# Optimization experiments

Measured on AMD Instinct MI355X. Metric: run time of the kernel, lower is better.

Reference implementation:

```python
import jax, jax.numpy as jnp
import numpy as np

TOP_K = 6
CAP_FACTOR = 2.0


def setup_inputs() -> dict:
    key = jax.random.key(0)
    ks = jax.random.split(key, 9)
    B, S, D, F, E, SH = 4, 2048, 512, 256, 64, 2
    return {
        "x": jax.random.normal(ks[0], (B, S, D), jnp.float32),
        "router_w": jax.random.normal(ks[1], (E, D), jnp.float32) * 0.02,
        "bias": jnp.zeros((E,), jnp.float32),
        "shared_w_gate": jax.random.normal(ks[2], (SH, F, D), jnp.float32) * 0.02,
        "shared_w_up": jax.random.normal(ks[3], (SH, F, D), jnp.float32) * 0.02,
        "shared_w_down": jax.random.normal(ks[4], (SH, D, F), jnp.float32) * 0.02,
        "w_gate": jax.random.normal(ks[5], (E, F, D), jnp.float32) * 0.02,
        "w_up": jax.random.normal(ks[6], (E, F, D), jnp.float32) * 0.02,
        "w_down": jax.random.normal(ks[7], (E, D, F), jnp.float32) * 0.02,
    }


def reference(x, router_w, bias, shared_w_gate, shared_w_up, shared_w_down, w_gate, w_up, w_down):
    B, S, D = x.shape
    E = router_w.shape[0]
    K = TOP_K
    N = B * S
    C = max(1, int(N * K * CAP_FACTOR / E))  # static per-expert capacity

    # Router logits with balancing bias (loop_idx=0 row).
    router_logits = jnp.einsum('bsd,ed->bse', x, router_w) + bias

    # Shared experts: averaged SwiGLU over SH experts, fully batched.
    hg = jnp.einsum('bsd,efd->bsef', x, shared_w_gate)
    hu = jnp.einsum('bsd,efd->bsef', x, shared_w_up)
    shared_out = jnp.einsum('bsef,edf->bsd', jax.nn.silu(hg) * hu, shared_w_down)
    shared_out = shared_out / shared_w_gate.shape[0]

    # Top-k routing, renormalised gates.
    router_probs = jax.nn.softmax(router_logits, axis=-1)
    topk_p, topk_i = jax.lax.top_k(router_probs, K)  # [B,S,K]
    topk_p = topk_p / (jnp.sum(topk_p, axis=-1, keepdims=True) + 1e-9)

    x_flat = x.reshape(N, D)
    flat_e = topk_i.reshape(-1)            # [N*K] expert ids
    flat_g = topk_p.reshape(-1)            # [N*K] gates
    token_ids = jnp.repeat(jnp.arange(N), K)

    # Stable sort by expert id -> contiguous expert groups.
    order = jnp.argsort(flat_e)            # jax argsort is stable
    se = flat_e[order]
    st = token_ids[order]
    sg = flat_g[order]

    M = se.shape[0]
    pos = jnp.arange(M)
    is_first = jnp.concatenate([jnp.ones((1,), bool), se[1:] != se[:-1]])
    group_starts = jax.lax.cummax(pos * is_first.astype(pos.dtype))
    slot = pos - group_starts              # position within expert group
    valid = slot < C                       # capacity drop
    safe_slot = jnp.where(valid, slot, C)  # overflow -> scratch slot C

    # Static-shape dispatch buffers (E, C+1, ...); slot C is scratch.
    expert_in = jnp.zeros((E, C + 1, D), x.dtype).at[se, safe_slot].set(x_flat[st])
    expert_gate = jnp.zeros((E, C + 1), x.dtype).at[se, safe_slot].set(sg)
    expert_tok = jnp.full((E, C + 1), N, jnp.int32).at[se, safe_slot].set(st.astype(jnp.int32))
    expert_mask = jnp.zeros((E, C + 1), bool).at[se, safe_slot].set(valid)

    expert_in = expert_in[:, :C]
    expert_gate = expert_gate[:, :C]
    expert_tok = expert_tok[:, :C]
    expert_mask = expert_mask[:, :C]

    # Grouped SwiGLU: three batched GEMMs over experts.
    hg = jnp.einsum('ecd,efd->ecf', expert_in, w_gate)
    hu = jnp.einsum('ecd,efd->ecf', expert_in, w_up)
    expert_out = jnp.einsum('ecf,edf->ecd', jax.nn.silu(hg) * hu, w_down)

    # Combine: scatter-add gated outputs back to tokens; row N is a sink.
    fm = expert_mask.reshape(-1)
    dst = jnp.where(fm, expert_tok.reshape(-1), N)
    fg = jnp.where(fm, expert_gate.reshape(-1), jnp.zeros((), x.dtype))
    sparse = jax.ops.segment_sum(fg[:, None] * expert_out.reshape(-1, D), dst, num_segments=N + 1)[:N]

    return shared_out + sparse.reshape(B, S, D)
```

## Files before the change

### kernel.cpp

```cpp
#include <hip/hip_runtime.h>
#include <hip/hip_bf16.h>
#include <math.h>

#define N_TOK 8192
#define D_DIM 512
#define F_DIM 256
#define E_NUM 64
#define SH_NUM 2
#define K_TOP 6
#define CAP   1536
#define M_ENT (N_TOK * K_TOP)
#define NCHUNK (M_ENT / 256)

#define EW_STRIDE 393216
#define E_TOT (E_NUM + SH_NUM)
#define X_BF_BYTES   (8388608ull)
#define WT_BYTES     ((size_t)E_TOT * EW_STRIDE * 2)
#define TOK_ROUTED   (E_NUM * CAP)
#define TOK_TOTAL    (TOK_ROUTED + SH_NUM * N_TOK)
#define EO_BYTES     ((size_t)TOK_TOTAL * D_DIM * 2)
#define RWT_BYTES    131072ull

#define SLOT 20480

typedef __attribute__((ext_vector_type(8))) short bf16x8;
typedef __attribute__((ext_vector_type(8))) short short8;
typedef __attribute__((ext_vector_type(4))) float f32x4;

#define VMCNT(n) asm volatile("s_waitcnt vmcnt(" #n ")" ::: "memory")

__device__ __forceinline__ ushort f2bf(float f) {
  union { float f; unsigned u; } c; c.f = f;
  return (ushort)((c.u + 0x7FFFu + ((c.u >> 16) & 1u)) >> 16);
}
__device__ __forceinline__ float bf2f(ushort h) {
  union { unsigned u; float f; } c; c.u = ((unsigned)h) << 16;
  return c.f;
}
__device__ __forceinline__ void gload16(const void* g, void* l) {
  __builtin_amdgcn_global_load_lds(
      (const __attribute__((address_space(1))) void*)g,
      (__attribute__((address_space(3))) void*)l, 16, 0, 0);
}

__global__ void router_topk(const float* __restrict__ x, const float* __restrict__ rw,
                            const float* __restrict__ bias, int* __restrict__ topk_i,
                            float* __restrict__ topk_p) {
  const int wave = threadIdx.x >> 6;
  const int lane = threadIdx.x & 63;
  const int n = blockIdx.x * 4 + wave;
  if (n >= N_TOK) return;

  const float4* xr = (const float4*)(x + (size_t)n * D_DIM);
  const float4* wr = (const float4*)(rw + (size_t)lane * D_DIM);
  float acc = 0.f;
  #pragma unroll 4
  for (int d4 = 0; d4 < D_DIM / 4; ++d4) {
    float4 xv = xr[d4]; float4 wv = wr[d4];
    acc += xv.x * wv.x + xv.y * wv.y + xv.z * wv.z + xv.w * wv.w;
  }
  float logit = acc + bias[lane];

  float m = logit;
  for (int off = 32; off > 0; off >>= 1) m = fmaxf(m, __shfl_xor(m, off));
  float p = expf(logit - m);
  float s = p;
  for (int off = 32; off > 0; off >>= 1) s += __shfl_xor(s, off);
  float prob = p / s;

  float myp = prob;
  float gsum = 0.f;
  float myg = 0.f; int myi = -1;
  for (int k = 0; k < K_TOP; ++k) {
    float bp = myp; int bi = lane;
    for (int off = 32; off > 0; off >>= 1) {
      float op = __shfl_xor(bp, off); int oi = __shfl_xor(bi, off);
      if (op > bp || (op == bp && oi < bi)) { bp = op; bi = oi; }
    }
    gsum += bp;
    if (lane == k) { myg = bp; myi = bi; }
    if (lane == bi) myp = -1.f;
  }
  if (lane < K_TOP) {
    topk_i[n * K_TOP + lane] = myi;
    topk_p[n * K_TOP + lane] = myg / (gsum + 1e-9f);
  }
}

__device__ __forceinline__ void softmax_topk_write(float logit, int n, int lane,
                                                   int* __restrict__ topk_i,
                                                   float* __restrict__ topk_p) {
  float m = logit;
  for (int off = 32; off > 0; off >>= 1) m = fmaxf(m, __shfl_xor(m, off));
  float p = expf(logit - m);
  float s = p;
  for (int off = 32; off > 0; off >>= 1) s += __shfl_xor(s, off);
  float prob = p / s;

  float myp = prob;
  float gsum = 0.f;
  float myg = 0.f; int myi = -1;
  #pragma unroll 1
  for (int k = 0; k < K_TOP; ++k) {
    float bp = myp; int bi = lane;
    for (int off = 32; off > 0; off >>= 1) {
      float op = __shfl_xor(bp, off); int oi = __shfl_xor(bi, off);
      if (op > bp || (op == bp && oi < bi)) { bp = op; bi = oi; }
    }
    gsum += bp;
    if (lane == k) { myg = bp; myi = bi; }
    if (lane == bi) myp = -1.f;
  }
  if (lane < K_TOP) {
    topk_i[n * K_TOP + lane] = myi;
    topk_p[n * K_TOP + lane] = myg / (gsum + 1e-9f);
  }
}

__global__ void __launch_bounds__(256) router_topk2(
    const float* __restrict__ x, const float* __restrict__ rwt,
    const float* __restrict__ bias, int* __restrict__ topk_i,
    float* __restrict__ topk_p) {
  const int wave = threadIdx.x >> 6;
  const int lane = threadIdx.x & 63;
  const int n0 = blockIdx.x * 32 + wave * 8;

  float acc[8];
  #pragma unroll
  for (int t = 0; t < 8; ++t) acc[t] = 0.f;

  const float4* wv4 = (const float4*)rwt;
  #pragma unroll 2
  for (int k4 = 0; k4 < 128; ++k4) {
    float4 w = wv4[k4 * 64 + lane];
    #pragma unroll
    for (int t = 0; t < 8; ++t) {
      float4 xv = *(const float4*)(x + (size_t)(n0 + t) * D_DIM + k4 * 4);
      acc[t] += xv.x * w.x + xv.y * w.y + xv.z * w.z + xv.w * w.w;
    }
  }
  float b = bias[lane];
  #pragma unroll 1
  for (int t = 0; t < 8; ++t)
    softmax_topk_write(acc[t] + b, n0 + t, lane, topk_i, topk_p);
}

__global__ void hist_kernel(const int* __restrict__ topk_i, int* __restrict__ chunk_hist) {
  __shared__ int h[E_NUM];
  const int tid = threadIdx.x;
  if (tid < E_NUM) h[tid] = 0;
  __syncthreads();
  int e = topk_i[blockIdx.x * 256 + tid];
  atomicAdd(&h[e], 1);
  __syncthreads();
  if (tid < E_NUM) chunk_hist[blockIdx.x * E_NUM + tid] = h[tid];
}

__global__ void scan_kernel(const int* __restrict__ chunk_hist, int* __restrict__ chunk_base) {
  const int e = threadIdx.x;
  int run = 0;
  for (int c = 0; c < NCHUNK; ++c) {
    chunk_base[c * E_NUM + e] = run;
    run += chunk_hist[c * E_NUM + e];
  }
}

__global__ void dispatch_kernel(const int* __restrict__ topk_i, const float* __restrict__ topk_p,
                                const int* __restrict__ chunk_base,
                                int* __restrict__ expert_tok, float* __restrict__ expert_gate,
                                int* __restrict__ entry_row) {
  __shared__ int eid[256];
  const int tid = threadIdx.x;
  const int m = blockIdx.x * 256 + tid;
  const int e = topk_i[m];
  eid[tid] = e;
  __syncthreads();
  int rank = 0;
  for (int t = 0; t < tid; ++t) rank += (eid[t] == e);
  int slot = chunk_base[blockIdx.x * E_NUM + e] + rank;
  int row = -1;
  if (slot < CAP) {
    expert_tok[e * CAP + slot] = m / K_TOP;
    expert_gate[e * CAP + slot] = topk_p[m];
    row = e * CAP + slot;
  }
  if (entry_row) entry_row[m] = row;
}


__global__ void convert_x_misc(const float* __restrict__ x, ushort* __restrict__ xb,
                               const float* __restrict__ rw, float* __restrict__ rwt,
                               int* __restrict__ tok_all, float* __restrict__ gate_all) {
  int b = blockIdx.x;
  if (b < 2048) {
    size_t idx = (size_t)b * 256 + threadIdx.x;
    const float4* s4 = (const float4*)(x + idx * 8);
    float4 v0 = s4[0], v1 = s4[1];
    short8 o;
    o[0] = f2bf(v0.x); o[1] = f2bf(v0.y); o[2] = f2bf(v0.z); o[3] = f2bf(v0.w);
    o[4] = f2bf(v1.x); o[5] = f2bf(v1.y); o[6] = f2bf(v1.z); o[7] = f2bf(v1.w);
    *(short8*)(xb + idx * 8) = o;
  } else if (b < 2080) {
    int idx = (b - 2048) * 256 + threadIdx.x;
    int e = idx >> 7, k4 = idx & 127;
    float4 v = *(const float4*)(rw + (size_t)e * D_DIM + k4 * 4);
    *(float4*)(rwt + ((size_t)k4 * 64 + e) * 4) = v;
  } else {
    int i = (b - 2080) * 256 + threadIdx.x;
    tok_all[TOK_ROUTED + i] = i & (N_TOK - 1);
    gate_all[TOK_ROUTED + i] = 0.5f;
  }
}

__global__ void convert_w(const float* __restrict__ wg_, const float* __restrict__ wu_,
                          const float* __restrict__ wd_, const float* __restrict__ swg,
                          const float* __restrict__ swu, const float* __restrict__ swd,
                          ushort* __restrict__ Wt) {
  int e = blockIdx.x / 12;
  int rem = blockIdx.x - e * 12;
  int p = rem >> 2, q = rem & 3;
  const float* src;
  if (p == 0)      src = (e < E_NUM) ? wg_ + (size_t)e * 131072 : swg + (size_t)(e - E_NUM) * 131072;
  else if (p == 1) src = (e < E_NUM) ? wu_ + (size_t)e * 131072 : swu + (size_t)(e - E_NUM) * 131072;
  else             src = (e < E_NUM) ? wd_ + (size_t)e * 131072 : swd + (size_t)(e - E_NUM) * 131072;
  ushort* dst = Wt + (size_t)e * EW_STRIDE + (size_t)p * 131072;
  #pragma unroll
  for (int i = 0; i < 16; ++i) {
    int d = q * 32768 + i * 2048 + threadIdx.x * 8;
    int ci = d >> 13;
    int r  = d & 8191;
    int nt = r >> 9;
    int rr = r & 511;
    int k8 = rr >> 7;
    int n  = nt * 16 + ((rr >> 3) & 15);
    size_t srcidx;
    if (p < 2) {
      srcidx = (size_t)n * 512 + ci * 32 + k8 * 8;
    } else {
      int np = ci >> 3, kc = ci & 7;
      srcidx = (size_t)(np * 256 + n) * 256 + kc * 32 + k8 * 8;
    }
    const float4* s4 = (const float4*)(src + srcidx);
    float4 v0 = s4[0], v1 = s4[1];
    short8 o;
    o[0] = f2bf(v0.x); o[1] = f2bf(v0.y); o[2] = f2bf(v0.z); o[3] = f2bf(v0.w);
    o[4] = f2bf(v1.x); o[5] = f2bf(v1.y); o[6] = f2bf(v1.z); o[7] = f2bf(v1.w);
    *(short8*)(dst + d) = o;
  }
}

template <bool GATHER>
__global__ void __launch_bounds__(512, 1) ffn_mfma(
    const ushort* __restrict__ xb, const ushort* __restrict__ Wt,
    const int* __restrict__ tok_all, const float* __restrict__ gate_all,
    float* __restrict__ out, ushort* __restrict__ expert_out) {
  int e, tbase;
  {
    int xcd = blockIdx.x & 7;
    int j = blockIdx.x >> 3;
    if (j < 96) {
      int ec = j / 12;
      int mt = j - ec * 12;
      e = ec * 8 + xcd;
      tbase = e * CAP + mt * 128;
      if (tok_all[tbase] < 0) return;
    } else {
      int s = xcd * 16 + (j - 96);
      int sh = s & 1, mt = s >> 1;
      e = E_NUM + sh;
      tbase = TOK_ROUTED + sh * N_TOK + mt * 128;
    }
  }
  const ushort* wbase = Wt + (size_t)e * EW_STRIDE;

  __shared__ ushort RING[2 * SLOT];
  __shared__ ushort Act[32768];
  __shared__ int   toks[128];
  __shared__ float gts[128];

  const int tid = threadIdx.x;
  const int lane = tid & 63;
  const int wid = tid >> 6;
  const int wr = wid >> 2;
  const int wc = wid & 3;
  const int rl = lane & 15;
  const int hi = lane >> 4;

  if (tid < 128) {
    int t = tok_all[tbase + tid];
    toks[tid] = t;
    gts[tid] = (t >= 0) ? gate_all[tbase + tid] : 0.f;
  }
  __syncthreads();

  int t0 = toks[wid * 16 + rl];
  const ushort* xsrc = xb + (size_t)(t0 < 0 ? 0 : t0) * D_DIM + hi * 8;

  auto stage_gu = [&](int sl, int kc) {
    ushort* dst = RING + sl * SLOT;
    gload16(xsrc + kc * 32, dst + wid * 512);
    #pragma unroll
    for (int i = 0; i < 2; ++i) {
      int s = wid * 2 + i;
      gload16(wbase + kc * 8192 + s * 512 + lane * 8, dst + 4096 + s * 512);
      gload16(wbase + 131072 + kc * 8192 + s * 512 + lane * 8, dst + 12288 + s * 512);
    }
  };
  auto stage_dn = [&](int sl, int kc) {
    ushort* dst = RING + sl * SLOT;
    #pragma unroll
    for (int i = 0; i < 4; ++i) {
      int s = wid * 4 + i;
      gload16(wbase + 262144 + (s >> 4) * 65536 + kc * 8192 + (s & 15) * 512 + lane * 8,
              dst + s * 512);
    }
  };

  const f32x4 fzero = {0.f, 0.f, 0.f, 0.f};
  f32x4 accg[4][4], accu[4][4];
  #pragma unroll
  for (int ri = 0; ri < 4; ++ri)
    #pragma unroll
    for (int bi = 0; bi < 4; ++bi) { accg[ri][bi] = fzero; accu[ri][bi] = fzero; }

  stage_gu(0, 0);
  {
    int sl = 0;
    #pragma unroll 1
    for (int kc = 0; kc < 16; ++kc) {
      if (kc < 15) { stage_gu(sl ^ 1, kc + 1); VMCNT(5); }
      else         VMCNT(0);
      __builtin_amdgcn_s_barrier();
      __builtin_amdgcn_sched_barrier(0);
      {
        const ushort* base = RING + sl * SLOT;
        bf16x8 a[4];
        #pragma unroll
        for (int ri = 0; ri < 4; ++ri)
          a[ri] = *(const bf16x8*)(base + (wr * 4 + ri) * 512 + lane * 8);
        __builtin_amdgcn_s_setprio(1);
        #pragma unroll
        for (int bi = 0; bi < 4; ++bi) {
          bf16x8 bg = *(const bf16x8*)(base + 4096 + (wc * 4 + bi) * 512 + lane * 8);
          bf16x8 bu = *(const bf16x8*)(base + 12288 + (wc * 4 + bi) * 512 + lane * 8);
          #pragma unroll
          for (int ri = 0; ri < 4; ++ri) {
            accg[ri][bi] = __builtin_amdgcn_mfma_f32_16x16x32_bf16(a[ri], bg, accg[ri][bi], 0, 0, 0);
            accu[ri][bi] = __builtin_amdgcn_mfma_f32_16x16x32_bf16(a[ri], bu, accu[ri][bi], 0, 0, 0);
          }
        }
        __builtin_amdgcn_s_setprio(0);
      }
      sl ^= 1;
      __builtin_amdgcn_s_barrier();
    }
  }

  #pragma unroll
  for (int ri = 0; ri < 4; ++ri)
    #pragma unroll
    for (int bi = 0; bi < 4; ++bi) {
      int st = (wr * 4 + ri) * 8 + wc * 2 + (bi >> 1);
      int base = st * 512 + ((bi & 1) * 2 + (rl >> 3)) * 128 + (rl & 7);
      #pragma unroll
      for (int j = 0; j < 4; ++j) {
        float g = accg[ri][bi][j], u = accu[ri][bi][j];
        Act[base + (hi * 4 + j) * 8] = f2bf(g / (1.f + __expf(-g)) * u);
      }
    }
  stage_dn(0, 0);
  __syncthreads();

  f32x4 accd[4][8];
  #pragma unroll
  for (int ri = 0; ri < 4; ++ri)
    #pragma unroll
    for (int bj = 0; bj < 8; ++bj) accd[ri][bj] = fzero;

  {
    int sl = 0;
    #pragma unroll 1
    for (int kc = 0; kc < 8; ++kc) {
      if (kc < 7) { stage_dn(sl ^ 1, kc + 1); VMCNT(4); }
      else        VMCNT(0);
      __builtin_amdgcn_s_barrier();
      __builtin_amdgcn_sched_barrier(0);
      {
        const ushort* base = RING + sl * SLOT;
        bf16x8 a[4];
        #pragma unroll
        for (int ri = 0; ri < 4; ++ri)
          a[ri] = *(const bf16x8*)(Act + ((wr * 4 + ri) * 8 + kc) * 512 + lane * 8);
        __builtin_amdgcn_s_setprio(1);
        #pragma unroll
        for (int bj = 0; bj < 8; ++bj) {
          bf16x8 b = *(const bf16x8*)(base + (wc >> 1) * 8192 + ((wc & 1) * 8 + bj) * 512 + lane * 8);
          #pragma unroll
          for (int ri = 0; ri < 4; ++ri)
            accd[ri][bj] = __builtin_amdgcn_mfma_f32_16x16x32_bf16(a[ri], b, accd[ri][bj], 0, 0, 0);
        }
        __builtin_amdgcn_s_setprio(0);
      }
      sl ^= 1;
      __builtin_amdgcn_s_barrier();
    }
  }

  if (GATHER) {
    #pragma unroll
    for (int ri = 0; ri < 4; ++ri)
      #pragma unroll
      for (int j = 0; j < 4; ++j) {
        int r = wr * 64 + ri * 16 + hi * 4 + j;
        if (toks[r] < 0) continue;
        ushort* erow = expert_out + (size_t)(tbase + r) * D_DIM + wc * 128 + rl;
        #pragma unroll
        for (int bj = 0; bj < 8; ++bj)
          erow[bj * 16] = f2bf(accd[ri][bj][j]);
      }
  } else {
    #pragma unroll
    for (int ri = 0; ri < 4; ++ri)
      #pragma unroll
      for (int j = 0; j < 4; ++j) {
        int r = wr * 64 + ri * 16 + hi * 4 + j;
        int t = toks[r];
        if (t < 0) continue;
        float gt = gts[r];
        float* orow = out + (size_t)t * D_DIM + wc * 128 + rl;
        #pragma unroll
        for (int bj = 0; bj < 8; ++bj)
          atomicAdd(orow + bj * 16, gt * accd[ri][bj][j]);
      }
  }
}

__global__ void __launch_bounds__(256) gather_out(
    const ushort* __restrict__ eo, const int* __restrict__ entry_row,
    const float* __restrict__ topk_p, float* __restrict__ out) {
  const int t = blockIdx.x * 4 + (threadIdx.x >> 6);
  const int lane = threadIdx.x & 63;
  const int base = t * K_TOP;

  float acc[8];
  #pragma unroll
  for (int j = 0; j < 8; ++j) acc[j] = 0.f;

  #pragma unroll
  for (int k = 0; k < K_TOP; ++k) {
    int row = entry_row[base + k];
    if (row >= 0) {
      float g = topk_p[base + k];
      bf16x8 v = *(const bf16x8*)(eo + (size_t)row * D_DIM + lane * 8);
      #pragma unroll
      for (int j = 0; j < 8; ++j) acc[j] += g * bf2f((ushort)v[j]);
    }
  }
  #pragma unroll
  for (int sh = 0; sh < SH_NUM; ++sh) {
    int row = TOK_ROUTED + sh * N_TOK + t;
    bf16x8 v = *(const bf16x8*)(eo + (size_t)row * D_DIM + lane * 8);
    #pragma unroll
    for (int j = 0; j < 8; ++j) acc[j] += 0.5f * bf2f((ushort)v[j]);
  }
  float4* o = (float4*)(out + (size_t)t * D_DIM + lane * 8);
  o[0] = make_float4(acc[0], acc[1], acc[2], acc[3]);
  o[1] = make_float4(acc[4], acc[5], acc[6], acc[7]);
}


__global__ void __launch_bounds__(256, 2) expert_ffn_mfma(
    const float* __restrict__ x, const float* __restrict__ wg_,
    const float* __restrict__ wu_, const float* __restrict__ wd_,
    const int* __restrict__ expert_tok, const float* __restrict__ expert_gate,
    float* __restrict__ out) {
  const int e = blockIdx.x & (E_NUM - 1);
  const int mt = blockIdx.x >> 6;
  const int s0 = mt * 64;
  if (expert_tok[e * CAP + s0] < 0) return;

  __shared__ ushort Xs[64][72];
  __shared__ ushort Ws[256][72];
  __shared__ ushort Act[64][264];
  __shared__ int   toks[64];
  __shared__ float gts[64];

  const int tid = threadIdx.x;
  const int lane = tid & 63;
  const int wid = tid >> 6;
  const int rl = lane & 15;
  const int ko = (lane >> 4) * 8;
  const int rquad = (lane >> 4) * 4;

  if (tid < 64) {
    int t = expert_tok[e * CAP + s0 + tid];
    toks[tid] = t;
    gts[tid] = (t >= 0) ? expert_gate[e * CAP + s0 + tid] : 0.f;
  }
  __syncthreads();

  float4 px[4], pw[16];

  auto loadX = [&](int kb) {
    #pragma unroll
    for (int it = 0; it < 4; ++it) {
      int idx = tid + it * 256;
      int row = idx >> 4, c4 = (idx & 15) << 2;
      int t = toks[row];
      px[it] = (t >= 0) ? *(const float4*)(x + (size_t)t * D_DIM + kb * 64 + c4)
                        : make_float4(0.f, 0.f, 0.f, 0.f);
    }
  };
  auto writeX = [&]() {
    #pragma unroll
    for (int it = 0; it < 4; ++it) {
      int idx = tid + it * 256;
      int row = idx >> 4, c4 = (idx & 15) << 2;
      ushort4 h; h.x = f2bf(px[it].x); h.y = f2bf(px[it].y);
      h.z = f2bf(px[it].z); h.w = f2bf(px[it].w);
      *(ushort4*)&Xs[row][c4] = h;
    }
  };
  auto loadW = [&](const float* src, int ldk, int kb) {
    #pragma unroll
    for (int it = 0; it < 16; ++it) {
      int idx = tid + it * 256;
      int row = idx >> 4, c4 = (idx & 15) << 2;
      pw[it] = *(const float4*)(src + (size_t)row * ldk + kb * 64 + c4);
    }
  };
  auto writeW = [&]() {
    #pragma unroll
    for (int it = 0; it < 16; ++it) {
      int idx = tid + it * 256;
      int row = idx >> 4, c4 = (idx & 15) << 2;
      ushort4 h; h.x = f2bf(pw[it].x); h.y = f2bf(pw[it].y);
      h.z = f2bf(pw[it].z); h.w = f2bf(pw[it].w);
      *(ushort4*)&Ws[row][c4] = h;
    }
  };
  auto compute = [&](const ushort* Ab, int lda, f32x4 (&acc)[4][4]) {
    #pragma unroll
    for (int kk = 0; kk < 2; ++kk) {
      bf16x8 a[4], b[4];
      #pragma unroll
      for (int ri = 0; ri < 4; ++ri)
        a[ri] = *(const bf16x8*)(Ab + (size_t)(ri * 16 + rl) * lda + kk * 32 + ko);
      #pragma unroll
      for (int bi = 0; bi < 4; ++bi)
        b[bi] = *(const bf16x8*)(&Ws[wid * 64 + bi * 16 + rl][kk * 32 + ko]);
      #pragma unroll
      for (int ri = 0; ri < 4; ++ri)
        #pragma unroll
        for (int bi = 0; bi < 4; ++bi)
          acc[ri][bi] = __builtin_amdgcn_mfma_f32_16x16x32_bf16(a[ri], b[bi], acc[ri][bi], 0, 0, 0);
    }
  };

  const f32x4 fzero = {0.f, 0.f, 0.f, 0.f};

  #pragma unroll 1
  for (int which = 0; which < 2; ++which) {
    const float* wsrc = (which == 0 ? wg_ : wu_) + (size_t)e * F_DIM * D_DIM;
    f32x4 acc[4][4];
    #pragma unroll
    for (int ri = 0; ri < 4; ++ri)
      #pragma unroll
      for (int bi = 0; bi < 4; ++bi) acc[ri][bi] = fzero;

    loadX(0); loadW(wsrc, D_DIM, 0);
    writeX(); writeW();
    __syncthreads();
    for (int kb = 0; kb < 8; ++kb) {
      if (kb < 7) { loadX(kb + 1); loadW(wsrc, D_DIM, kb + 1); }
      compute(&Xs[0][0], 72, acc);
      __syncthreads();
      if (kb < 7) { writeX(); writeW(); __syncthreads(); }
    }
    #pragma unroll
    for (int ri = 0; ri < 4; ++ri)
      #pragma unroll
      for (int bi = 0; bi < 4; ++bi)
        #pragma unroll
        for (int j = 0; j < 4; ++j) {
          int r = ri * 16 + rquad + j;
          int c = wid * 64 + bi * 16 + rl;
          if (which == 0) {
            Act[r][c] = f2bf(acc[ri][bi][j]);
          } else {
            float hg = bf2f(Act[r][c]);
            float a = hg / (1.f + __expf(-hg)) * acc[ri][bi][j];
            Act[r][c] = f2bf(a);
          }
        }
    __syncthreads();
  }

  #pragma unroll 1
  for (int np = 0; np < 2; ++np) {
    const float* wsrc = wd_ + ((size_t)e * D_DIM + np * 256) * F_DIM;
    f32x4 acc[4][4];
    #pragma unroll
    for (int ri = 0; ri < 4; ++ri)
      #pragma unroll
      for (int bi = 0; bi < 4; ++bi) acc[ri][bi] = fzero;

    loadW(wsrc, F_DIM, 0); writeW();
    __syncthreads();
    for (int kb = 0; kb < 4; ++kb) {
      if (kb < 3) loadW(wsrc, F_DIM, kb + 1);
      compute(&Act[0][kb * 64], 264, acc);
      __syncthreads();
      if (kb < 3) { writeW(); __syncthreads(); }
    }
    #pragma unroll
    for (int ri = 0; ri < 4; ++ri)
      #pragma unroll
      for (int bi = 0; bi < 4; ++bi)
        #pragma unroll
        for (int j = 0; j < 4; ++j) {
          int r = ri * 16 + rquad + j;
          int t = toks[r];
          if (t >= 0) {
            int c = np * 256 + wid * 64 + bi * 16 + rl;
            atomicAdd(out + (size_t)t * D_DIM + c, gts[r] * acc[ri][bi][j]);
          }
        }
  }
}

__global__ void __launch_bounds__(256, 2) shared_ffn_mfma(
    const float* __restrict__ x, const float* __restrict__ swg,
    const float* __restrict__ swu, const float* __restrict__ swd,
    float* __restrict__ out) {
  const int row0 = blockIdx.x * 32;

  __shared__ ushort Xs[32][72];
  __shared__ ushort Ws[256][72];
  __shared__ ushort Act[32][264];

  const int tid = threadIdx.x;
  const int lane = tid & 63;
  const int wid = tid >> 6;
  const int rl = lane & 15;
  const int ko = (lane >> 4) * 8;
  const int rquad = (lane >> 4) * 4;

  float4 px[2], pw[16];

  auto loadX = [&](int kb) {
    #pragma unroll
    for (int it = 0; it < 2; ++it) {
      int idx = tid + it * 256;
      int row = idx >> 4, c4 = (idx & 15) << 2;
      px[it] = *(const float4*)(x + (size_t)(row0 + row) * D_DIM + kb * 64 + c4);
    }
  };
  auto writeX = [&]() {
    #pragma unroll
    for (int it = 0; it < 2; ++it) {
      int idx = tid + it * 256;
      int row = idx >> 4, c4 = (idx & 15) << 2;
      ushort4 h; h.x = f2bf(px[it].x); h.y = f2bf(px[it].y);
      h.z = f2bf(px[it].z); h.w = f2bf(px[it].w);
      *(ushort4*)&Xs[row][c4] = h;
    }
  };
  auto loadW = [&](const float* src, int ldk, int kb) {
    #pragma unroll
    for (int it = 0; it < 16; ++it) {
      int idx = tid + it * 256;
      int row = idx >> 4, c4 = (idx & 15) << 2;
      pw[it] = *(const float4*)(src + (size_t)row * ldk + kb * 64 + c4);
    }
  };
  auto writeW = [&]() {
    #pragma unroll
    for (int it = 0; it < 16; ++it) {
      int idx = tid + it * 256;
      int row = idx >> 4, c4 = (idx & 15) << 2;
      ushort4 h; h.x = f2bf(pw[it].x); h.y = f2bf(pw[it].y);
      h.z = f2bf(pw[it].z); h.w = f2bf(pw[it].w);
      *(ushort4*)&Ws[row][c4] = h;
    }
  };
  auto compute = [&](const ushort* Ab, int lda, f32x4 (&acc)[2][4]) {
    #pragma unroll
    for (int kk = 0; kk < 2; ++kk) {
      bf16x8 a[2], b[4];
      #pragma unroll
      for (int ri = 0; ri < 2; ++ri)
        a[ri] = *(const bf16x8*)(Ab + (size_t)(ri * 16 + rl) * lda + kk * 32 + ko);
      #pragma unroll
      for (int bi = 0; bi < 4; ++bi)
        b[bi] = *(const bf16x8*)(&Ws[wid * 64 + bi * 16 + rl][kk * 32 + ko]);
      #pragma unroll
      for (int ri = 0; ri < 2; ++ri)
        #pragma unroll
        for (int bi = 0; bi < 4; ++bi)
          acc[ri][bi] = __builtin_amdgcn_mfma_f32_16x16x32_bf16(a[ri], b[bi], acc[ri][bi], 0, 0, 0);
    }
  };

  const f32x4 fzero = {0.f, 0.f, 0.f, 0.f};
  f32x4 accd[2][2][4];
  #pragma unroll
  for (int np = 0; np < 2; ++np)
    #pragma unroll
    for (int ri = 0; ri < 2; ++ri)
      #pragma unroll
      for (int bi = 0; bi < 4; ++bi) accd[np][ri][bi] = fzero;

  #pragma unroll 1
  for (int sh = 0; sh < SH_NUM; ++sh) {
    #pragma unroll 1
    for (int which = 0; which < 2; ++which) {
      const float* wsrc = (which == 0 ? swg : swu) + (size_t)sh * F_DIM * D_DIM;
      f32x4 acc[2][4];
      #pragma unroll
      for (int ri = 0; ri < 2; ++ri)
        #pragma unroll
        for (int bi = 0; bi < 4; ++bi) acc[ri][bi] = fzero;

      loadX(0); loadW(wsrc, D_DIM, 0);
      writeX(); writeW();
      __syncthreads();
      for (int kb = 0; kb < 8; ++kb) {
        if (kb < 7) { loadX(kb + 1); loadW(wsrc, D_DIM, kb + 1); }
        compute(&Xs[0][0], 72, acc);
        __syncthreads();
        if (kb < 7) { writeX(); writeW(); __syncthreads(); }
      }
      #pragma unroll
      for (int ri = 0; ri < 2; ++ri)
        #pragma unroll
        for (int bi = 0; bi < 4; ++bi)
          #pragma unroll
          for (int j = 0; j < 4; ++j) {
            int r = ri * 16 + rquad + j;
            int c = wid * 64 + bi * 16 + rl;
            if (which == 0) {
              Act[r][c] = f2bf(acc[ri][bi][j]);
            } else {
              float hg = bf2f(Act[r][c]);
              float a = hg / (1.f + __expf(-hg)) * acc[ri][bi][j];
              Act[r][c] = f2bf(a);
            }
          }
      __syncthreads();
    }
    #pragma unroll
    for (int np = 0; np < 2; ++np) {
      const float* wsrc = swd + ((size_t)sh * D_DIM + np * 256) * F_DIM;
      loadW(wsrc, F_DIM, 0); writeW();
      __syncthreads();
      for (int kb = 0; kb < 4; ++kb) {
        if (kb < 3) loadW(wsrc, F_DIM, kb + 1);
        compute(&Act[0][kb * 64], 264, accd[np]);
        __syncthreads();
        if (kb < 3) { writeW(); __syncthreads(); }
      }
    }
  }

  #pragma unroll
  for (int np = 0; np < 2; ++np)
    #pragma unroll
    for (int ri = 0; ri < 2; ++ri)
      #pragma unroll
      for (int bi = 0; bi < 4; ++bi)
        #pragma unroll
        for (int j = 0; j < 4; ++j) {
          int r = ri * 16 + rquad + j;
          int c = np * 256 + wid * 64 + bi * 16 + rl;
          out[(size_t)(row0 + r) * D_DIM + c] = 0.5f * accd[np][ri][bi][j];
        }
}

extern "C" void kernel_launch(void* const* d_in, const int* in_sizes, int n_in,
                              void* d_out, int out_size, void* d_ws, size_t ws_size,
                              hipStream_t stream) {
  const float* x    = (const float*)d_in[0];
  const float* rw   = (const float*)d_in[1];
  const float* bias = (const float*)d_in[2];
  const float* swg  = (const float*)d_in[3];
  const float* swu  = (const float*)d_in[4];
  const float* swd  = (const float*)d_in[5];
  const float* wg   = (const float*)d_in[6];
  const float* wu   = (const float*)d_in[7];
  const float* wd   = (const float*)d_in[8];
  float* out = (float*)d_out;

  const size_t small = 2 * (size_t)M_ENT * 4 + (size_t)M_ENT * 4 +
                       2 * (size_t)NCHUNK * E_NUM * 4 + 2 * (size_t)TOK_TOTAL * 4 +
                       RWT_BYTES;
  const size_t need_mid = X_BF_BYTES + WT_BYTES + small;
  const size_t need_big = need_mid + EO_BYTES;

  if (ws_size >= need_mid) {
    const bool gather = (ws_size >= need_big);
    char* ws = (char*)d_ws;
    ushort* x_bf     = (ushort*)ws; ws += X_BF_BYTES;
    ushort* Wt       = (ushort*)ws; ws += WT_BYTES;
    int*   topk_i    = (int*)ws;    ws += (size_t)M_ENT * 4;
    float* topk_p    = (float*)ws;  ws += (size_t)M_ENT * 4;
    int*   entry_row = (int*)ws;    ws += (size_t)M_ENT * 4;
    int*   chunk_hist= (int*)ws;    ws += (size_t)NCHUNK * E_NUM * 4;
    int*   chunk_base= (int*)ws;    ws += (size_t)NCHUNK * E_NUM * 4;
    int*   tok_all   = (int*)ws;    ws += (size_t)TOK_TOTAL * 4;
    float* gate_all  = (float*)ws;  ws += (size_t)TOK_TOTAL * 4;
    float* rwt       = (float*)ws;  ws += RWT_BYTES;
    ushort* eo       = (ushort*)ws;

    convert_x_misc<<<2144, 256, 0, stream>>>(x, x_bf, rw, rwt, tok_all, gate_all);
    convert_w<<<E_TOT * 12, 256, 0, stream>>>(wg, wu, wd, swg, swu, swd, Wt);
    router_topk2<<<256, 256, 0, stream>>>(x, rwt, bias, topk_i, topk_p);
    hipMemsetAsync(tok_all, 0xFF, (size_t)TOK_ROUTED * 4, stream);
    if (!gather) hipMemsetAsync(out, 0, (size_t)out_size * 4, stream);
    hist_kernel<<<NCHUNK, 256, 0, stream>>>(topk_i, chunk_hist);
    scan_kernel<<<1, 64, 0, stream>>>(chunk_hist, chunk_base);
    dispatch_kernel<<<NCHUNK, 256, 0, stream>>>(topk_i, topk_p, chunk_base, tok_all,
                                                gate_all, entry_row);
    const int nblk = (CAP / 128) * E_NUM + 2 * (N_TOK / 128);
    if (gather) {
      ffn_mfma<true><<<nblk, 512, 0, stream>>>(x_bf, Wt, tok_all, gate_all, out, eo);
      gather_out<<<N_TOK / 4, 256, 0, stream>>>(eo, entry_row, topk_p, out);
    } else {
      ffn_mfma<false><<<nblk, 512, 0, stream>>>(x_bf, Wt, tok_all, gate_all, out, nullptr);
    }
  } else {
    char* ws = (char*)d_ws;
    int*   topk_i      = (int*)ws;   ws += (size_t)M_ENT * 4;
    float* topk_p      = (float*)ws; ws += (size_t)M_ENT * 4;
    int*   chunk_hist  = (int*)ws;   ws += (size_t)NCHUNK * E_NUM * 4;
    int*   chunk_base  = (int*)ws;   ws += (size_t)NCHUNK * E_NUM * 4;
    int*   expert_tok  = (int*)ws;   ws += (size_t)E_NUM * CAP * 4;
    float* expert_gate = (float*)ws; ws += (size_t)E_NUM * CAP * 4;

    router_topk<<<N_TOK / 4, 256, 0, stream>>>(x, rw, bias, topk_i, topk_p);
    hipMemsetAsync(expert_tok, 0xFF, (size_t)E_NUM * CAP * 4, stream);
    hist_kernel<<<NCHUNK, 256, 0, stream>>>(topk_i, chunk_hist);
    scan_kernel<<<1, 64, 0, stream>>>(chunk_hist, chunk_base);
    dispatch_kernel<<<NCHUNK, 256, 0, stream>>>(topk_i, topk_p, chunk_base, expert_tok,
                                                expert_gate, nullptr);
    shared_ffn_mfma<<<N_TOK / 32, 256, 0, stream>>>(x, swg, swu, swd, out);
    expert_ffn_mfma<<<(CAP / 64) * E_NUM, 256, 0, stream>>>(x, wg, wu, wd, expert_tok,
                                                            expert_gate, out);
  }
}
```

Baseline: 262.1 us.

## Load expert weights directly into registers instead of staging through LDS

The gate/up and down-projection weight tiles are now read straight from global memory into VGPRs with register double-buffering, and only the token activations still go through a smaller LDS ring. The down-projection loop drops its barriers and relies on register prefetch of the next chunk. This is meant to remove LDS write/read traffic and shrink LDS use, possibly allowing more occupancy. In exchange it raises register pressure considerably, and since each wave loads its own weight slice, weights are reread more often across waves with less coalescing reuse.

Result: faster. 254.3 us (-3.0%).

```diff
diff --git a/kernel.cpp b/kernel.cpp
--- a/kernel.cpp
+++ b/kernel.cpp
@@ -20,8 +20,6 @@
 #define TOK_TOTAL    (TOK_ROUTED + SH_NUM * N_TOK)
 #define EO_BYTES     ((size_t)TOK_TOTAL * D_DIM * 2)
 #define RWT_BYTES    131072ull
-
-#define SLOT 20480
 
 typedef __attribute__((ext_vector_type(8))) short bf16x8;
 typedef __attribute__((ext_vector_type(8))) short short8;
@@ -273,7 +271,7 @@
   }
   const ushort* wbase = Wt + (size_t)e * EW_STRIDE;
 
-  __shared__ ushort RING[2 * SLOT];
+  __shared__ ushort XR[2][4096];
   __shared__ ushort Act[32768];
   __shared__ int   toks[128];
   __shared__ float gts[128];
@@ -296,23 +294,15 @@
   int t0 = toks[wid * 16 + rl];
   const ushort* xsrc = xb + (size_t)(t0 < 0 ? 0 : t0) * D_DIM + hi * 8;
 
-  auto stage_gu = [&](int sl, int kc) {
-    ushort* dst = RING + sl * SLOT;
-    gload16(xsrc + kc * 32, dst + wid * 512);
-    #pragma unroll
-    for (int i = 0; i < 2; ++i) {
-      int s = wid * 2 + i;
-      gload16(wbase + kc * 8192 + s * 512 + lane * 8, dst + 4096 + s * 512);
-      gload16(wbase + 131072 + kc * 8192 + s * 512 + lane * 8, dst + 12288 + s * 512);
-    }
-  };
-  auto stage_dn = [&](int sl, int kc) {
-    ushort* dst = RING + sl * SLOT;
-    #pragma unroll
-    for (int i = 0; i < 4; ++i) {
-      int s = wid * 4 + i;
-      gload16(wbase + 262144 + (s >> 4) * 65536 + kc * 8192 + (s & 15) * 512 + lane * 8,
-              dst + s * 512);
+  auto stageX = [&](int sl, int kc) {
+    gload16(xsrc + kc * 32, &XR[sl][wid * 512]);
+  };
+  auto loadW = [&](int kc, bf16x8 (&g)[4], bf16x8 (&u)[4]) {
+    #pragma unroll
+    for (int bi = 0; bi < 4; ++bi) {
+      const ushort* p = wbase + kc * 8192 + (wc * 4 + bi) * 512 + lane * 8;
+      g[bi] = *(const bf16x8*)p;
+      u[bi] = *(const bf16x8*)(p + 131072);
     }
   };
 
@@ -323,35 +313,53 @@
     #pragma unroll
     for (int bi = 0; bi < 4; ++bi) { accg[ri][bi] = fzero; accu[ri][bi] = fzero; }
 
-  stage_gu(0, 0);
-  {
-    int sl = 0;
-    #pragma unroll 1
-    for (int kc = 0; kc < 16; ++kc) {
-      if (kc < 15) { stage_gu(sl ^ 1, kc + 1); VMCNT(5); }
-      else         VMCNT(0);
+  bf16x8 gA[4], uA[4], gB[4], uB[4];
+
+  auto guMFMA = [&](int sl, bf16x8 (&g)[4], bf16x8 (&u)[4]) {
+    bf16x8 a[4];
+    #pragma unroll
+    for (int ri = 0; ri < 4; ++ri)
+      a[ri] = *(const bf16x8*)(&XR[sl][(wr * 4 + ri) * 512 + lane * 8]);
+    __builtin_amdgcn_s_setprio(1);
+    #pragma unroll
+    for (int bi = 0; bi < 4; ++bi)
+      #pragma unroll
+      for (int ri = 0; ri < 4; ++ri) {
+        accg[ri][bi] = __builtin_amdgcn_mfma_f32_16x16x32_bf16(a[ri], g[bi], accg[ri][bi], 0, 0, 0);
+        accu[ri][bi] = __builtin_amdgcn_mfma_f32_16x16x32_bf16(a[ri], u[bi], accu[ri][bi], 0, 0, 0);
+      }
+    __builtin_amdgcn_s_setprio(0);
+  };
+
+  loadW(0, gA, uA); stageX(0, 0);
+  __builtin_amdgcn_sched_barrier(0);
+  VMCNT(0);
+  __builtin_amdgcn_s_barrier();
+
+  #pragma unroll 1
+  for (int k2 = 0; k2 < 16; k2 += 2) {
+    {
+      const int k = k2;
+      if (k < 15) {
+        loadW(k + 1, gB, uB); stageX((k + 1) & 1, k + 1);
+        __builtin_amdgcn_sched_barrier(0);
+        VMCNT(9);
+      } else { __builtin_amdgcn_sched_barrier(0); VMCNT(0); }
       __builtin_amdgcn_s_barrier();
       __builtin_amdgcn_sched_barrier(0);
-      {
-        const ushort* base = RING + sl * SLOT;
-        bf16x8 a[4];
-        #pragma unroll
-        for (int ri = 0; ri < 4; ++ri)
-          a[ri] = *(const bf16x8*)(base + (wr * 4 + ri) * 512 + lane * 8);
-        __builtin_amdgcn_s_setprio(1);
-        #pragma unroll
-        for (int bi = 0; bi < 4; ++bi) {
-          bf16x8 bg = *(const bf16x8*)(base + 4096 + (wc * 4 + bi) * 512 + lane * 8);
-          bf16x8 bu = *(const bf16x8*)(base + 12288 + (wc * 4 + bi) * 512 + lane * 8);
-          #pragma unroll
-          for (int ri = 0; ri < 4; ++ri) {
-            accg[ri][bi] = __builtin_amdgcn_mfma_f32_16x16x32_bf16(a[ri], bg, accg[ri][bi], 0, 0, 0);
-            accu[ri][bi] = __builtin_amdgcn_mfma_f32_16x16x32_bf16(a[ri], bu, accu[ri][bi], 0, 0, 0);
-          }
-        }
-        __builtin_amdgcn_s_setprio(0);
-      }
-      sl ^= 1;
+      guMFMA(0, gA, uA);
+      __builtin_amdgcn_s_barrier();
+    }
+    {
+      const int k = k2 + 1;
+      if (k < 15) {
+        loadW(k + 1, gA, uA); stageX((k + 1) & 1, k + 1);
+        __builtin_amdgcn_sched_barrier(0);
+        VMCNT(9);
+      } else { __builtin_amdgcn_sched_barrier(0); VMCNT(0); }
+      __builtin_amdgcn_s_barrier();
+      __builtin_amdgcn_sched_barrier(0);
+      guMFMA(1, gB, uB);
       __builtin_amdgcn_s_barrier();
     }
   }
@@ -368,42 +376,44 @@
         Act[base + (hi * 4 + j) * 8] = f2bf(g / (1.f + __expf(-g)) * u);
       }
     }
-  stage_dn(0, 0);
+
+  const ushort* wdbase = wbase + 262144 + (wc >> 1) * 65536 + ((wc & 1) * 8) * 512 + lane * 8;
+  auto loadWd = [&](int kc, bf16x8 (&d)[8]) {
+    #pragma unroll
+    for (int bj = 0; bj < 8; ++bj)
+      d[bj] = *(const bf16x8*)(wdbase + kc * 8192 + bj * 512);
+  };
+
+  f32x4 accd[4][8];
+  #pragma unroll
+  for (int ri = 0; ri < 4; ++ri)
+    #pragma unroll
+    for (int bj = 0; bj < 8; ++bj) accd[ri][bj] = fzero;
+
+  bf16x8 dA[8], dB[8];
+  loadWd(0, dA);
   __syncthreads();
 
-  f32x4 accd[4][8];
-  #pragma unroll
-  for (int ri = 0; ri < 4; ++ri)
-    #pragma unroll
-    for (int bj = 0; bj < 8; ++bj) accd[ri][bj] = fzero;
-
-  {
-    int sl = 0;
-    #pragma unroll 1
-    for (int kc = 0; kc < 8; ++kc) {
-      if (kc < 7) { stage_dn(sl ^ 1, kc + 1); VMCNT(4); }
-      else        VMCNT(0);
-      __builtin_amdgcn_s_barrier();
-      __builtin_amdgcn_sched_barrier(0);
-      {
-        const ushort* base = RING + sl * SLOT;
-        bf16x8 a[4];
-        #pragma unroll
-        for (int ri = 0; ri < 4; ++ri)
-          a[ri] = *(const bf16x8*)(Act + ((wr * 4 + ri) * 8 + kc) * 512 + lane * 8);
-        __builtin_amdgcn_s_setprio(1);
-        #pragma unroll
-        for (int bj = 0; bj < 8; ++bj) {
-          bf16x8 b = *(const bf16x8*)(base + (wc >> 1) * 8192 + ((wc & 1) * 8 + bj) * 512 + lane * 8);
-          #pragma unroll
-          for (int ri = 0; ri < 4; ++ri)
-            accd[ri][bj] = __builtin_amdgcn_mfma_f32_16x16x32_bf16(a[ri], b, accd[ri][bj], 0, 0, 0);
-        }
-        __builtin_amdgcn_s_setprio(0);
-      }
-      sl ^= 1;
-      __builtin_amdgcn_s_barrier();
-    }
+  auto dnMFMA = [&](int kc, bf16x8 (&d)[8]) {
+    bf16x8 a[4];
+    #pragma unroll
+    for (int ri = 0; ri < 4; ++ri)
+      a[ri] = *(const bf16x8*)(&Act[((wr * 4 + ri) * 8 + kc) * 512 + lane * 8]);
+    __builtin_amdgcn_s_setprio(1);
+    #pragma unroll
+    for (int bj = 0; bj < 8; ++bj)
+      #pragma unroll
+      for (int ri = 0; ri < 4; ++ri)
+        accd[ri][bj] = __builtin_amdgcn_mfma_f32_16x16x32_bf16(a[ri], d[bj], accd[ri][bj], 0, 0, 0);
+    __builtin_amdgcn_s_setprio(0);
+  };
+
+  #pragma unroll 1
+  for (int k2 = 0; k2 < 8; k2 += 2) {
+    loadWd(k2 + 1, dB);
+    dnMFMA(k2, dA);
+    if (k2 + 2 < 8) loadWd(k2 + 2, dA);
+    dnMFMA(k2 + 1, dB);
   }
 
   if (GATHER) {
```
